# Optimization experiments

Hardware: AMD Instinct MI355X
Metric: run time of the kernel (lower is better)

The kernel has to match this reference:

```python
import jax, jax.numpy as jnp
import numpy as np

B, NP, J, C, H, W, L = 16, 64, 17, 480, 128, 128, 4
EPS = 1e-5
COCO_EDGES = [(15,13),(13,11),(16,14),(14,12),(11,12),(5,11),(6,12),(5,6),(5,7),(6,8),(7,9),(8,10),(1,2),(0,1),(0,2),(1,3),(2,4),(3,5),(4,6)]

def build_adj():
    g = np.eye(J, dtype=np.float32)
    for a, b in COCO_EDGES:
        g[a, b] = 1.0
        g[b, a] = 1.0
    r = g.sum(1) ** -0.5  # symmetric normalization D^-1/2 A D^-1/2
    return jnp.asarray(r[:, None] * g * r[None, :])

def make_bn(k):
    ks = jax.random.split(k, 4)
    gamma = 1.0 + 0.1 * jax.random.normal(ks[0], (C,))
    beta = 0.1 * jax.random.normal(ks[1], (C,))
    mean = 0.1 * jax.random.normal(ks[2], (C,))
    var = 0.5 + jax.random.uniform(ks[3], (C,))
    return jnp.stack([gamma, beta, mean, var])  # [4, C]

def setup_inputs() -> dict:
    key = jax.random.key(0)
    ks = jax.random.split(key, 12)
    s = 0.02
    features = jax.random.normal(ks[0], (B, C, H, W), jnp.float32)
    coords = jax.random.uniform(ks[1], (B, NP, J, 2)) * jnp.array([W - 1.0, H - 1.0], jnp.float32)
    center_ind = jax.random.randint(ks[2], (B, NP), 0, H * W)
    bn_res = jax.vmap(make_bn)(jax.random.split(ks[3], L * 2)).reshape(L, 2, 4, C)
    return {
        'features': features,
        'coords': coords,
        'center_ind': center_ind,
        'adj': build_adj(),
        'Wh': s * jax.random.normal(ks[4], (C, C)),
        'bh': jnp.zeros((C,)),
        'bn_head': make_bn(ks[5]),
        'Wres': s * jax.random.normal(ks[6], (L, 2, C, C)),
        'bres': jnp.zeros((L, 2, C)),
        'bn_res': bn_res,
        'Wp1': s * jax.random.normal(ks[7], (C, 3 * C)),
        'bp1': jnp.zeros((C,)),
        'bn_pred': make_bn(ks[8]),
        'Wp2': s * jax.random.normal(ks[9], (2 * J, C)),
        'bp2': jnp.zeros((2 * J,)),
    }

def _bn(x, p):
    # eval-mode BatchNorm1d over the channel (last) axis; p = [gamma, beta, mean, var]
    return (x - p[2]) * jax.lax.rsqrt(p[3] + EPS) * p[0] + p[1]

def _gblock(x, adj, Wt, bt, p):
    # graph conv (adj @ (x W) + b) -> BN -> ReLU ; x: [N, J, C]
    return jax.nn.relu(_bn(jnp.einsum('jk,nkc->njc', adj, x @ Wt) + bt, p))

_gat = jax.vmap(lambda f, i: f[:, i])  # f: [C, HW], i: int idx -> [C, *i.shape]

def reference(features, coords, center_ind, adj, Wh, bh, bn_head, Wres, bres, bn_res, Wp1, bp1, bn_pred, Wp2, bp2):
    flat = features.reshape(B, C, H * W)
    # --- float_sample: bilinear sampling of per-joint features ---
    x, y = coords[..., 0], coords[..., 1]
    x0f = jnp.clip(jnp.floor(x), 0.0, W - 2.0)
    y0f = jnp.clip(jnp.floor(y), 0.0, H - 2.0)
    x0 = x0f.astype(jnp.int32)
    y0 = y0f.astype(jnp.int32)
    wx = (x - x0f)[:, None]  # [B,1,NP,J]
    wy = (y - y0f)[:, None]
    i00 = y0 * W + x0
    f00 = _gat(flat, i00)
    f01 = _gat(flat, i00 + 1)
    f10 = _gat(flat, i00 + W)
    f11 = _gat(flat, i00 + W + 1)
    fj = f00 * (1 - wx) * (1 - wy) + f01 * wx * (1 - wy) + f10 * (1 - wx) * wy + f11 * wx * wy  # [B,C,NP,J]
    feat_joints = jnp.transpose(fj, (0, 2, 3, 1)).reshape(B * NP, J, C)
    # --- int_sample: center features ---
    feat_center = jnp.transpose(_gat(flat, center_ind), (0, 2, 1))  # [B,NP,C]
    # --- stacked graph conv blocks ---
    h = _gblock(feat_joints, adj, Wh, bh, bn_head)
    for i in range(L):
        res = h
        h = _gblock(h, adj, Wres[i, 0], bres[i, 0], bn_res[i, 0])
        h = _gblock(h, adj, Wres[i, 1], bres[i, 1], bn_res[i, 1])
        h = res + h
    f1 = h.mean(axis=1).reshape(B, NP, C)
    f2 = h.max(axis=1).reshape(B, NP, C)
    feats = jnp.concatenate([f1, f2, feat_center], axis=-1)  # [B,NP,3C]
    p = jax.nn.relu(_bn(feats @ Wp1.T + bp1, bn_pred))  # 1x1 conv + BN + ReLU
    return p @ Wp2.T + bp2  # [B, NP, 2*J] refine offsets
```

## Files before the change

### kernel.cpp

```cpp
#include <hip/hip_runtime.h>
#include <math.h>

#define B_    16
#define NP_   64
#define J_    17
#define C_    480
#define H_    128
#define W_    128
#define L_    4
#define HW_   (H_ * W_)
#define NSAMP (B_ * NP_)
#define MROWS (NSAMP * J_)
#define EPS_  1e-5f
#define NMAT  (1 + 2 * L_)
#define NPAD  512
#define TC    96
#define TS    64
#define NT_   (256 * 5 * B_)
#define NW_   11520

typedef __attribute__((ext_vector_type(8))) short bf16x8;
typedef __attribute__((ext_vector_type(4))) short bf16x4;
typedef __attribute__((ext_vector_type(4))) float f32x4;

__device__ __forceinline__ unsigned short f2bf(float f) {
    unsigned int u = __float_as_uint(f);
    unsigned int r = (u + 0x7fffu + ((u >> 16) & 1u)) >> 16;
    return (unsigned short)r;
}
__device__ __forceinline__ float bf2f(unsigned short h) {
    return __uint_as_float(((unsigned int)h) << 16);
}

#define GLD16(gsrc, ldst)                                                                 \
    __builtin_amdgcn_global_load_lds((const __attribute__((address_space(1))) void*)(gsrc), \
                                     (__attribute__((address_space(3))) void*)(ldst), 16, 0, 0)

__global__ __launch_bounds__(256) void k_prep(const float* __restrict__ feat,
                                              const float* __restrict__ Wh,
                                              const float* __restrict__ Wres,
                                              const float* __restrict__ Wp1,
                                              short* __restrict__ nhwc,
                                              short* __restrict__ WtH,
                                              short* __restrict__ WpH) {
    int bid = blockIdx.x;
    int tid = threadIdx.x;
    if (bid < NT_) {
        __shared__ float t[TC][73];
        int sb = bid & 255;
        int cb = (bid >> 8) % 5;
        int b  = bid / 1280;
        int c0 = cb * TC, s0 = sb * TS;
        const float* src = feat + ((size_t)b * C_ + c0) * HW_ + s0;
        #pragma unroll
        for (int i = 0; i < 6; ++i) {
            int f  = tid + i * 256;
            int c  = f >> 4;
            int sq = (f & 15) * 4;
            float4 v = *reinterpret_cast<const float4*>(src + (size_t)c * HW_ + sq);
            t[c][sq + 0] = v.x;
            t[c][sq + 1] = v.y;
            t[c][sq + 2] = v.z;
            t[c][sq + 3] = v.w;
        }
        __syncthreads();
        int sy = tid >> 2;
        int cx = (tid & 3) * (TC / 4);
        short* dst = nhwc + ((size_t)b * HW_ + s0 + sy) * C_ + c0 + cx;
        alignas(16) unsigned short tmp[TC / 4];
        #pragma unroll
        for (int i = 0; i < TC / 4; ++i) tmp[i] = f2bf(t[cx + i][sy]);
        #pragma unroll
        for (int i = 0; i < 3; ++i)
            *reinterpret_cast<uint4*>(dst + i * 8) = *reinterpret_cast<const uint4*>(tmp + i * 8);
    } else {
        int gid = (bid - NT_) * 256 + tid;
        const int t1 = NMAT * NPAD * C_;
        const int t2 = NPAD * 3 * C_;
        if (gid < t1) {
            int m   = gid / (NPAD * C_);
            int rem = gid % (NPAD * C_);
            int n = rem / C_;
            int k = rem % C_;
            float v = 0.f;
            if (n < C_) {
                const float* src = (m == 0) ? Wh : (Wres + (size_t)(m - 1) * C_ * C_);
                v = src[(size_t)k * C_ + n];
            }
            WtH[gid] = (short)f2bf(v);
        } else if (gid < t1 + t2) {
            int g2 = gid - t1;
            int n = g2 / (3 * C_);
            int k = g2 % (3 * C_);
            float v = (n < C_) ? Wp1[(size_t)n * 3 * C_ + k] : 0.f;
            WpH[g2] = (short)f2bf(v);
        }
    }
}

__global__ __launch_bounds__(256) void k_gather_mix(const short* __restrict__ nhwc,
                                                    const float* __restrict__ coords,
                                                    const float* __restrict__ adj,
                                                    short* __restrict__ Ah) {
    __shared__ float sX[J_][C_];
    __shared__ float sadj[J_ * J_];
    __shared__ float sw[J_][4];
    __shared__ int   si[J_];
    int n = blockIdx.x;
    int b = n / NP_;
    for (int t = threadIdx.x; t < J_ * J_; t += 256) sadj[t] = adj[t];
    if (threadIdx.x < J_) {
        int j = threadIdx.x;
        int p = n * J_ + j;
        float x = coords[p * 2 + 0];
        float y = coords[p * 2 + 1];
        float x0f = fminf(fmaxf(floorf(x), 0.f), (float)(W_ - 2));
        float y0f = fminf(fmaxf(floorf(y), 0.f), (float)(H_ - 2));
        float wx = x - x0f, wy = y - y0f;
        sw[j][0] = (1.f - wx) * (1.f - wy);
        sw[j][1] = wx * (1.f - wy);
        sw[j][2] = (1.f - wx) * wy;
        sw[j][3] = wx * wy;
        si[j] = (int)y0f * W_ + (int)x0f;
    }
    __syncthreads();
    const short* base = nhwc + (size_t)b * HW_ * C_;
    for (int idx = threadIdx.x; idx < J_ * (C_ / 8); idx += 256) {
        int j  = idx / (C_ / 8);
        int c8 = (idx - j * (C_ / 8)) * 8;
        const short* p00 = base + (size_t)si[j] * C_ + c8;
        bf16x8 v00 = *reinterpret_cast<const bf16x8*>(p00);
        bf16x8 v01 = *reinterpret_cast<const bf16x8*>(p00 + C_);
        bf16x8 v10 = *reinterpret_cast<const bf16x8*>(p00 + W_ * C_);
        bf16x8 v11 = *reinterpret_cast<const bf16x8*>(p00 + W_ * C_ + C_);
        float w0 = sw[j][0], w1 = sw[j][1], w2 = sw[j][2], w3 = sw[j][3];
        #pragma unroll
        for (int e = 0; e < 8; ++e) {
            sX[j][c8 + e] = bf2f((unsigned short)v00[e]) * w0 +
                            bf2f((unsigned short)v01[e]) * w1 +
                            bf2f((unsigned short)v10[e]) * w2 +
                            bf2f((unsigned short)v11[e]) * w3;
        }
    }
    __syncthreads();
    size_t obase = (size_t)n * J_ * C_;
    for (int c = threadIdx.x; c < C_; c += 256) {
        float xv[J_];
        #pragma unroll
        for (int k = 0; k < J_; k++) xv[k] = sX[k][c];
        #pragma unroll
        for (int j = 0; j < J_; j++) {
            float s = 0.f;
            #pragma unroll
            for (int k = 0; k < J_; k++) s += sadj[j * J_ + k] * xv[k];
            Ah[obase + (size_t)j * C_ + c] = (short)f2bf(s);
        }
    }
}

__global__ __launch_bounds__(256) void k_mix_bf16(const short* __restrict__ Xin,
                                                  const float* __restrict__ adj,
                                                  short* __restrict__ Ah) {
    __shared__ float sadj[J_ * J_];
    for (int t = threadIdx.x; t < J_ * J_; t += 256) sadj[t] = adj[t];
    __syncthreads();
    int t = threadIdx.x;
    if (t >= 240) return;
    int n  = blockIdx.x * 2 + (t / 120);
    int c4 = (t % 120) * 4;
    const short* xb = Xin + (size_t)n * J_ * C_ + c4;
    float xf[J_][4];
    #pragma unroll
    for (int k = 0; k < J_; k++) {
        bf16x4 v = *reinterpret_cast<const bf16x4*>(xb + (size_t)k * C_);
        #pragma unroll
        for (int e = 0; e < 4; ++e) xf[k][e] = bf2f((unsigned short)v[e]);
    }
    short* yb = Ah + (size_t)n * J_ * C_ + c4;
    #pragma unroll
    for (int j = 0; j < J_; j++) {
        float a0 = 0.f, a1 = 0.f, a2 = 0.f, a3 = 0.f;
        #pragma unroll
        for (int k = 0; k < J_; k++) {
            float w = sadj[j * J_ + k];
            a0 = fmaf(w, xf[k][0], a0);
            a1 = fmaf(w, xf[k][1], a1);
            a2 = fmaf(w, xf[k][2], a2);
            a3 = fmaf(w, xf[k][3], a3);
        }
        bf16x4 o = {(short)f2bf(a0), (short)f2bf(a1), (short)f2bf(a2), (short)f2bf(a3)};
        *reinterpret_cast<bf16x4*>(yb + (size_t)j * C_) = o;
    }
}

template <bool ADD>
__global__ __launch_bounds__(256) void k_gemm_mfma(const short* __restrict__ A,
                                                   const short* __restrict__ Bm,
                                                   const float* __restrict__ bias,
                                                   const float* __restrict__ bn4,
                                                   const short* res,
                                                   short* out,
                                                   int M, int N, int K) {
    __shared__ short lds[2 * 6144];

    int nwg = gridDim.x * gridDim.y;
    int lin = blockIdx.y * gridDim.x + blockIdx.x;
    int cpx = nwg >> 3;
    int swz = (lin & 7) * cpx + (lin >> 3);
    const int row0 = (swz / gridDim.x) * 64;
    const int col0 = (swz % gridDim.x) * 128;

    const int tid  = threadIdx.x;
    const int lane = tid & 63;
    const int wid  = tid >> 6;
    const int wm0  = (wid >> 1) * 32;
    const int wn0  = (wid & 1) * 64;

    f32x4 acc[2][4];
    #pragma unroll
    for (int i = 0; i < 2; i++)
        #pragma unroll
        for (int j = 0; j < 4; j++) acc[i][j] = (f32x4){0.f, 0.f, 0.f, 0.f};

    const int kq = lane >> 4;
    const int fr = lane & 15;

    int rA, cqA, rB[2], cqB[2];
    {
        int p = wid * 1024 + lane * 16;
        int v = p >> 6;
        rA  = v ^ ((v >> 2) & 1);
        cqA = ((p >> 4) & 3) ^ (rA & 3);
    }
    #pragma unroll
    for (int t = 0; t < 2; ++t) {
        int p = (2 * wid + t) * 1024 + lane * 16;
        int v = p >> 6;
        int r = v ^ ((v >> 2) & 1);
        rB[t]  = r;
        cqB[t] = ((p >> 4) & 3) ^ (r & 3);
    }
    const short* pA  = A  + (size_t)(row0 + rA) * K + cqA * 8;
    const short* pB0 = Bm + (size_t)(col0 + rB[0]) * K + cqB[0] * 8;
    const short* pB1 = Bm + (size_t)(col0 + rB[1]) * K + cqB[1] * 8;
    const int aA  = wid * 1024;
    const int aB0 = 4096 + (2 * wid + 0) * 1024;
    const int aB1 = 4096 + (2 * wid + 1) * 1024;

    const int NS = K / 32;
    {
        char* lb = (char*)lds;
        GLD16(pA, lb + aA);
        GLD16(pB0, lb + aB0);
        GLD16(pB1, lb + aB1);
    }
    __syncthreads();

    for (int ks = 0; ks < NS; ++ks) {
        if (ks + 1 < NS) {
            const int kk = (ks + 1) * 32;
            char* lb = (char*)lds + ((ks + 1) & 1) * 12288;
            GLD16(pA + kk, lb + aA);
            GLD16(pB0 + kk, lb + aB0);
            GLD16(pB1 + kk, lb + aB1);
        }
        const short* lbc = lds + (ks & 1) * 6144;
        bf16x8 fa[2], fb[4];
        #pragma unroll
        for (int mf = 0; mf < 2; ++mf) {
            int r  = wm0 + mf * 16 + fr;
            int so = ((r * 64 + kq * 16) ^ ((r & 7) << 4)) >> 1;
            fa[mf] = *reinterpret_cast<const bf16x8*>(lbc + so);
        }
        #pragma unroll
        for (int nf = 0; nf < 4; ++nf) {
            int r  = wn0 + nf * 16 + fr;
            int so = ((r * 64 + kq * 16) ^ ((r & 7) << 4)) >> 1;
            fb[nf] = *reinterpret_cast<const bf16x8*>(lbc + 2048 + so);
        }
        __builtin_amdgcn_s_setprio(1);
        #pragma unroll
        for (int mf = 0; mf < 2; ++mf)
            #pragma unroll
            for (int nf = 0; nf < 4; ++nf)
                acc[mf][nf] = __builtin_amdgcn_mfma_f32_16x16x32_bf16(fa[mf], fb[nf], acc[mf][nf], 0, 0, 0);
        __builtin_amdgcn_s_setprio(0);
        __syncthreads();
    }

    const int rq = lane >> 4;
    #pragma unroll
    for (int nf = 0; nf < 4; ++nf) {
        int col = col0 + wn0 + nf * 16 + fr;
        if (col >= N) continue;
        float bia = bias[col];
        float g   = bn4[col];
        float be  = bn4[N + col];
        float mu  = bn4[2 * N + col];
        float va  = bn4[3 * N + col];
        float sc  = rsqrtf(va + EPS_) * g;
        #pragma unroll
        for (int mf = 0; mf < 2; ++mf) {
            #pragma unroll
            for (int r = 0; r < 4; ++r) {
                int row = row0 + wm0 + mf * 16 + rq * 4 + r;
                float v = acc[mf][nf][r] + bia;
                v = (v - mu) * sc + be;
                v = fmaxf(v, 0.f);
                if (ADD) v += bf2f((unsigned short)res[(size_t)row * N + col]);
                out[(size_t)row * N + col] = (short)f2bf(v);
            }
        }
    }
}

__global__ __launch_bounds__(256) void k_pool(const short* __restrict__ Hb,
                                              const short* __restrict__ nhwc,
                                              const int* __restrict__ cidx,
                                              short* __restrict__ feats) {
    int n = blockIdx.x;
    int b = n / NP_;
    const short* cen = nhwc + ((size_t)b * HW_ + cidx[n]) * C_;
    for (int c = threadIdx.x; c < C_; c += 256) {
        float s = 0.f, m = -INFINITY;
        #pragma unroll
        for (int j = 0; j < J_; j++) {
            float v = bf2f((unsigned short)Hb[((size_t)n * J_ + j) * C_ + c]);
            s += v;
            m = fmaxf(m, v);
        }
        feats[(size_t)n * 3 * C_ + c]          = (short)f2bf(s * (1.f / (float)J_));
        feats[(size_t)n * 3 * C_ + C_ + c]     = (short)f2bf(m);
        feats[(size_t)n * 3 * C_ + 2 * C_ + c] = cen[c];
    }
}

__global__ __launch_bounds__(256) void k_final(const short* __restrict__ P,
                                               const float* __restrict__ W2,
                                               const float* __restrict__ b2,
                                               float* __restrict__ out) {
    int g = blockIdx.x * 256 + threadIdx.x;
    if (g >= NSAMP * 2 * J_) return;
    int m = g / (2 * J_);
    int o = g % (2 * J_);
    const short* pr = P + (size_t)m * C_;
    const float* wr = W2 + (size_t)o * C_;
    float s = 0.f;
    for (int k = 0; k < C_; k += 4) {
        s = fmaf(bf2f((unsigned short)pr[k + 0]), wr[k + 0], s);
        s = fmaf(bf2f((unsigned short)pr[k + 1]), wr[k + 1], s);
        s = fmaf(bf2f((unsigned short)pr[k + 2]), wr[k + 2], s);
        s = fmaf(bf2f((unsigned short)pr[k + 3]), wr[k + 3], s);
    }
    out[g] = s + b2[o];
}

extern "C" void kernel_launch(void* const* d_in, const int* in_sizes, int n_in,
                              void* d_out, int out_size, void* d_ws, size_t ws_size,
                              hipStream_t stream) {
    const float* features = (const float*)d_in[0];
    const float* coords   = (const float*)d_in[1];
    const int*   center   = (const int*)d_in[2];
    const float* adj      = (const float*)d_in[3];
    const float* Wh       = (const float*)d_in[4];
    const float* bh       = (const float*)d_in[5];
    const float* bn_head  = (const float*)d_in[6];
    const float* Wres     = (const float*)d_in[7];
    const float* bres     = (const float*)d_in[8];
    const float* bn_res   = (const float*)d_in[9];
    const float* Wp1      = (const float*)d_in[10];
    const float* bp1      = (const float*)d_in[11];
    const float* bn_pred  = (const float*)d_in[12];
    const float* Wp2      = (const float*)d_in[13];
    const float* bp2      = (const float*)d_in[14];
    float* out = (float*)d_out;

    char* ws = (char*)d_ws;
    short* nhwc  = (short*)ws;   ws += (size_t)B_ * HW_ * C_ * 2;
    short* bufX  = (short*)ws;   ws += (size_t)MROWS * C_ * 2;
    short* bufH  = (short*)ws;   ws += (size_t)MROWS * C_ * 2;
    short* AhB   = (short*)ws;   ws += (size_t)MROWS * C_ * 2;
    short* featsB= (short*)ws;   ws += (size_t)NSAMP * 3 * C_ * 2;
    short* bufP  = (short*)ws;   ws += (size_t)NSAMP * C_ * 2;
    short* WtH   = (short*)ws;   ws += (size_t)NMAT * NPAD * C_ * 2;
    short* WpH   = (short*)ws;   ws += (size_t)NPAD * 3 * C_ * 2;

    dim3 gg(4, MROWS / 64);
    dim3 gp(4, NSAMP / 64);

    k_prep<<<NT_ + NW_, 256, 0, stream>>>(features, Wh, Wres, Wp1, nhwc, WtH, WpH);

    k_gather_mix<<<NSAMP, 256, 0, stream>>>(nhwc, coords, adj, AhB);
    k_gemm_mfma<false><<<gg, 256, 0, stream>>>(AhB, WtH, bh, bn_head,
                                               nullptr, bufH, MROWS, C_, C_);

    for (int i = 0; i < L_; i++) {
        int m1 = 1 + 2 * i, m2 = 2 + 2 * i;
        k_mix_bf16<<<NSAMP / 2, 256, 0, stream>>>(bufH, adj, AhB);
        k_gemm_mfma<false><<<gg, 256, 0, stream>>>(
            AhB, WtH + (size_t)m1 * NPAD * C_,
            bres + (size_t)(2 * i) * C_, bn_res + (size_t)(2 * i) * 4 * C_,
            nullptr, bufX, MROWS, C_, C_);
        k_mix_bf16<<<NSAMP / 2, 256, 0, stream>>>(bufX, adj, AhB);
        k_gemm_mfma<true><<<gg, 256, 0, stream>>>(
            AhB, WtH + (size_t)m2 * NPAD * C_,
            bres + (size_t)(2 * i + 1) * C_, bn_res + (size_t)(2 * i + 1) * 4 * C_,
            bufH, bufH, MROWS, C_, C_);
    }

    k_pool<<<NSAMP, 256, 0, stream>>>(bufH, nhwc, center, featsB);

    k_gemm_mfma<false><<<gp, 256, 0, stream>>>(featsB, WpH, bp1, bn_pred,
                                               nullptr, bufP, NSAMP, C_, 3 * C_);

    k_final<<<(NSAMP * 2 * J_ + 255) / 256, 256, 0, stream>>>(bufP, Wp2, bp2, out);
}
```

Measured before the change: 574.2 us.

## Fuse adjacency mixing into GEMM epilogue with sample-aligned 68-row tiles

Removes the separate adjacency-mix kernels by computing X·W first and applying the 17x17 adjacency in the GEMM epilogue. Each block now covers 4 whole samples (68 rows) so the mix stays inside the tile, which is staged through an LDS panel. This saves a full activation round trip to global memory and one launch per layer. In exchange the M tile is odd-sized (80 rows computed for 68 used), the epilogue is heavier, and rounding changes because the mix now runs in fp32 after the GEMM rather than before it.

```diff
diff --git a/kernel.cpp b/kernel.cpp
--- a/kernel.cpp
+++ b/kernel.cpp
@@ -18,6 +18,7 @@
 #define TS    64
 #define NT_   (256 * 5 * B_)
 #define NW_   11520
+#define PSTR  133
 
 typedef __attribute__((ext_vector_type(8))) short bf16x8;
 typedef __attribute__((ext_vector_type(4))) short bf16x4;
@@ -98,17 +99,13 @@
     }
 }
 
-__global__ __launch_bounds__(256) void k_gather_mix(const short* __restrict__ nhwc,
-                                                    const float* __restrict__ coords,
-                                                    const float* __restrict__ adj,
-                                                    short* __restrict__ Ah) {
-    __shared__ float sX[J_][C_];
-    __shared__ float sadj[J_ * J_];
+__global__ __launch_bounds__(256) void k_gather(const short* __restrict__ nhwc,
+                                                const float* __restrict__ coords,
+                                                short* __restrict__ Xs) {
     __shared__ float sw[J_][4];
     __shared__ int   si[J_];
     int n = blockIdx.x;
     int b = n / NP_;
-    for (int t = threadIdx.x; t < J_ * J_; t += 256) sadj[t] = adj[t];
     if (threadIdx.x < J_) {
         int j = threadIdx.x;
         int p = n * J_ + j;
@@ -134,62 +131,151 @@
         bf16x8 v10 = *reinterpret_cast<const bf16x8*>(p00 + W_ * C_);
         bf16x8 v11 = *reinterpret_cast<const bf16x8*>(p00 + W_ * C_ + C_);
         float w0 = sw[j][0], w1 = sw[j][1], w2 = sw[j][2], w3 = sw[j][3];
+        bf16x8 o;
         #pragma unroll
         for (int e = 0; e < 8; ++e) {
-            sX[j][c8 + e] = bf2f((unsigned short)v00[e]) * w0 +
-                            bf2f((unsigned short)v01[e]) * w1 +
-                            bf2f((unsigned short)v10[e]) * w2 +
-                            bf2f((unsigned short)v11[e]) * w3;
-        }
+            float v = bf2f((unsigned short)v00[e]) * w0 +
+                      bf2f((unsigned short)v01[e]) * w1 +
+                      bf2f((unsigned short)v10[e]) * w2 +
+                      bf2f((unsigned short)v11[e]) * w3;
+            o[e] = (short)f2bf(v);
+        }
+        *reinterpret_cast<bf16x8*>(Xs + ((size_t)n * J_ + j) * C_ + c8) = o;
+    }
+}
+
+template <bool ADD>
+__global__ __launch_bounds__(256) void k_fgemm(const short* __restrict__ X,
+                                               const short* __restrict__ Bm,
+                                               const float* __restrict__ adj,
+                                               const float* __restrict__ bias,
+                                               const float* __restrict__ bn4,
+                                               const short* res,
+                                               short* out,
+                                               int K) {
+    __shared__ __align__(16) char smem[80 * PSTR * 4];
+    __shared__ float sadj[J_ * J_];
+
+    int nwg = gridDim.x * gridDim.y;
+    int lin = blockIdx.y * gridDim.x + blockIdx.x;
+    int cpx = nwg >> 3;
+    int swz = (lin & 7) * cpx + (lin >> 3);
+    const int rb   = swz / gridDim.x;
+    const int cb   = swz % gridDim.x;
+    const int row0 = rb * 68;
+    const int col0 = cb * 128;
+
+    const int tid  = threadIdx.x;
+    const int lane = tid & 63;
+    const int wid  = tid >> 6;
+    const int wn0  = wid * 32;
+    const int kq   = lane >> 4;
+    const int fr   = lane & 15;
+
+    for (int t = tid; t < J_ * J_; t += 256) sadj[t] = adj[t];
+
+    f32x4 acc[5][2];
+    #pragma unroll
+    for (int i = 0; i < 5; i++)
+        #pragma unroll
+        for (int j = 0; j < 2; j++) acc[i][j] = (f32x4){0.f, 0.f, 0.f, 0.f};
+
+    const short* psrc[4];
+    int lof[4];
+    #pragma unroll
+    for (int t = 0; t < 4; ++t) {
+        int sl = (wid == 0) ? t : (1 + 3 * wid + t);
+        if (sl > 12) sl = 12;
+        int isA  = (sl < 5);
+        int prel = (isA ? sl : sl - 5) * 1024 + lane * 16;
+        int v = prel >> 6;
+        int r = v ^ ((v >> 2) & 1);
+        int cq = ((prel >> 4) & 3) ^ (r & 3);
+        psrc[t] = isA ? (X + (size_t)(row0 + r) * K + cq * 8)
+                      : (Bm + (size_t)(col0 + r) * K + cq * 8);
+        lof[t] = sl * 1024;
+    }
+
+    const int NS = K / 32;
+    {
+        char* lb = smem;
+        #pragma unroll
+        for (int t = 0; t < 4; ++t)
+            if (t < 3 || wid == 0) GLD16(psrc[t], lb + lof[t]);
     }
     __syncthreads();
-    size_t obase = (size_t)n * J_ * C_;
-    for (int c = threadIdx.x; c < C_; c += 256) {
-        float xv[J_];
-        #pragma unroll
-        for (int k = 0; k < J_; k++) xv[k] = sX[k][c];
-        #pragma unroll
-        for (int j = 0; j < J_; j++) {
+
+    for (int ks = 0; ks < NS; ++ks) {
+        if (ks + 1 < NS) {
+            const int kk = (ks + 1) * 32;
+            char* lb = smem + ((ks + 1) & 1) * 13312;
+            #pragma unroll
+            for (int t = 0; t < 4; ++t)
+                if (t < 3 || wid == 0) GLD16(psrc[t] + kk, lb + lof[t]);
+        }
+        const short* lbc = (const short*)(smem + (ks & 1) * 13312);
+        bf16x8 fa[5], fb[2];
+        #pragma unroll
+        for (int mf = 0; mf < 5; ++mf) {
+            int r  = mf * 16 + fr;
+            int so = ((r * 64 + kq * 16) ^ ((r & 7) << 4)) >> 1;
+            fa[mf] = *reinterpret_cast<const bf16x8*>(lbc + so);
+        }
+        #pragma unroll
+        for (int nf = 0; nf < 2; ++nf) {
+            int r  = wn0 + nf * 16 + fr;
+            int so = ((r * 64 + kq * 16) ^ ((r & 7) << 4)) >> 1;
+            fb[nf] = *reinterpret_cast<const bf16x8*>(lbc + 2560 + so);
+        }
+        __builtin_amdgcn_s_setprio(1);
+        #pragma unroll
+        for (int mf = 0; mf < 5; ++mf)
+            #pragma unroll
+            for (int nf = 0; nf < 2; ++nf)
+                acc[mf][nf] = __builtin_amdgcn_mfma_f32_16x16x32_bf16(fa[mf], fb[nf], acc[mf][nf], 0, 0, 0);
+        __builtin_amdgcn_s_setprio(0);
+        __syncthreads();
+    }
+
+    float* panel = (float*)smem;
+    const int rq = lane >> 4;
+    #pragma unroll
+    for (int mf = 0; mf < 5; ++mf)
+        #pragma unroll
+        for (int nf = 0; nf < 2; ++nf) {
+            int colp = wn0 + nf * 16 + fr;
+            int rowp = mf * 16 + rq * 4;
+            #pragma unroll
+            for (int rr = 0; rr < 4; ++rr)
+                panel[(rowp + rr) * PSTR + colp] = acc[mf][nf][rr];
+        }
+    __syncthreads();
+
+    for (int wi = tid; wi < 512; wi += 256) {
+        int si = wi >> 7;
+        int c  = wi & 127;
+        int col = col0 + c;
+        if (col >= C_) continue;
+        float ys[J_];
+        #pragma unroll
+        for (int j = 0; j < J_; ++j) ys[j] = panel[(si * J_ + j) * PSTR + c];
+        float bia = bias[col];
+        float g  = bn4[col];
+        float be = bn4[C_ + col];
+        float mu = bn4[2 * C_ + col];
+        float va = bn4[3 * C_ + col];
+        float sc = rsqrtf(va + EPS_) * g;
+        size_t gbase = (size_t)(row0 + si * J_) * C_ + col;
+        #pragma unroll
+        for (int j = 0; j < J_; ++j) {
             float s = 0.f;
             #pragma unroll
-            for (int k = 0; k < J_; k++) s += sadj[j * J_ + k] * xv[k];
-            Ah[obase + (size_t)j * C_ + c] = (short)f2bf(s);
-        }
-    }
-}
-
-__global__ __launch_bounds__(256) void k_mix_bf16(const short* __restrict__ Xin,
-                                                  const float* __restrict__ adj,
-                                                  short* __restrict__ Ah) {
-    __shared__ float sadj[J_ * J_];
-    for (int t = threadIdx.x; t < J_ * J_; t += 256) sadj[t] = adj[t];
-    __syncthreads();
-    int t = threadIdx.x;
-    if (t >= 240) return;
-    int n  = blockIdx.x * 2 + (t / 120);
-    int c4 = (t % 120) * 4;
-    const short* xb = Xin + (size_t)n * J_ * C_ + c4;
-    float xf[J_][4];
-    #pragma unroll
-    for (int k = 0; k < J_; k++) {
-        bf16x4 v = *reinterpret_cast<const bf16x4*>(xb + (size_t)k * C_);
-        #pragma unroll
-        for (int e = 0; e < 4; ++e) xf[k][e] = bf2f((unsigned short)v[e]);
-    }
-    short* yb = Ah + (size_t)n * J_ * C_ + c4;
-    #pragma unroll
-    for (int j = 0; j < J_; j++) {
-        float a0 = 0.f, a1 = 0.f, a2 = 0.f, a3 = 0.f;
-        #pragma unroll
-        for (int k = 0; k < J_; k++) {
-            float w = sadj[j * J_ + k];
-            a0 = fmaf(w, xf[k][0], a0);
-            a1 = fmaf(w, xf[k][1], a1);
-            a2 = fmaf(w, xf[k][2], a2);
-            a3 = fmaf(w, xf[k][3], a3);
-        }
-        bf16x4 o = {(short)f2bf(a0), (short)f2bf(a1), (short)f2bf(a2), (short)f2bf(a3)};
-        *reinterpret_cast<bf16x4*>(yb + (size_t)j * C_) = o;
+            for (int k = 0; k < J_; ++k) s = fmaf(sadj[j * J_ + k], ys[k], s);
+            float v = (s + bia - mu) * sc + be;
+            v = fmaxf(v, 0.f);
+            if (ADD) v += bf2f((unsigned short)res[gbase + (size_t)j * C_]);
+            out[gbase + (size_t)j * C_] = (short)f2bf(v);
+        }
     }
 }
 
@@ -375,37 +461,36 @@
     const float* bp2      = (const float*)d_in[14];
     float* out = (float*)d_out;
 
+    const size_t ACT = (size_t)(MROWS + 16) * C_ * 2;
     char* ws = (char*)d_ws;
     short* nhwc  = (short*)ws;   ws += (size_t)B_ * HW_ * C_ * 2;
-    short* bufX  = (short*)ws;   ws += (size_t)MROWS * C_ * 2;
-    short* bufH  = (short*)ws;   ws += (size_t)MROWS * C_ * 2;
-    short* AhB   = (short*)ws;   ws += (size_t)MROWS * C_ * 2;
+    short* bufS  = (short*)ws;   ws += ACT;
+    short* bufX  = (short*)ws;   ws += ACT;
+    short* bufH  = (short*)ws;   ws += ACT;
     short* featsB= (short*)ws;   ws += (size_t)NSAMP * 3 * C_ * 2;
     short* bufP  = (short*)ws;   ws += (size_t)NSAMP * C_ * 2;
     short* WtH   = (short*)ws;   ws += (size_t)NMAT * NPAD * C_ * 2;
     short* WpH   = (short*)ws;   ws += (size_t)NPAD * 3 * C_ * 2;
 
-    dim3 gg(4, MROWS / 64);
+    dim3 gf(4, NSAMP / 4);
     dim3 gp(4, NSAMP / 64);
 
     k_prep<<<NT_ + NW_, 256, 0, stream>>>(features, Wh, Wres, Wp1, nhwc, WtH, WpH);
-
-    k_gather_mix<<<NSAMP, 256, 0, stream>>>(nhwc, coords, adj, AhB);
-    k_gemm_mfma<false><<<gg, 256, 0, stream>>>(AhB, WtH, bh, bn_head,
-                                               nullptr, bufH, MROWS, C_, C_);
+    k_gather<<<NSAMP, 256, 0, stream>>>(nhwc, coords, bufS);
+
+    k_fgemm<false><<<gf, 256, 0, stream>>>(bufS, WtH, adj, bh, bn_head,
+                                           nullptr, bufH, C_);
 
     for (int i = 0; i < L_; i++) {
         int m1 = 1 + 2 * i, m2 = 2 + 2 * i;
-        k_mix_bf16<<<NSAMP / 2, 256, 0, stream>>>(bufH, adj, AhB);
-        k_gemm_mfma<false><<<gg, 256, 0, stream>>>(
-            AhB, WtH + (size_t)m1 * NPAD * C_,
+        k_fgemm<false><<<gf, 256, 0, stream>>>(
+            bufH, WtH + (size_t)m1 * NPAD * C_, adj,
             bres + (size_t)(2 * i) * C_, bn_res + (size_t)(2 * i) * 4 * C_,
-            nullptr, bufX, MROWS, C_, C_);
-        k_mix_bf16<<<NSAMP / 2, 256, 0, stream>>>(bufX, adj, AhB);
-        k_gemm_mfma<true><<<gg, 256, 0, stream>>>(
-            AhB, WtH + (size_t)m2 * NPAD * C_,
+            nullptr, bufX, C_);
+        k_fgemm<true><<<gf, 256, 0, stream>>>(
+            bufX, WtH + (size_t)m2 * NPAD * C_, adj,
             bres + (size_t)(2 * i + 1) * C_, bn_res + (size_t)(2 * i + 1) * 4 * C_,
-            bufH, bufH, MROWS, C_, C_);
+            bufH, bufH, C_);
     }
 
     k_pool<<<NSAMP, 256, 0, stream>>>(bufH, nhwc, center, featsB);
```

New measurement: 828.3 us. 44.2% more time.
